# Performance work log

Measured on AMD Instinct MI355X. Metric: run time of the kernel, lower is better.

The kernel has to match this reference:

```python
import jax, jax.numpy as jnp
import numpy as np

HIDDEN = 1024
HEADS = 16
HEAD_DIM = HIDDEN // HEADS


def setup_inputs() -> dict:
    key = jax.random.key(0)
    ks = jax.random.split(key, 11)
    B, S = 2, 2048
    s = 1.0 / np.sqrt(HIDDEN)
    return {
        "query": jax.random.normal(ks[0], (B, S, HIDDEN), jnp.float32),
        "key": jax.random.normal(ks[1], (B, S, HIDDEN), jnp.float32),
        "value": jax.random.normal(ks[2], (B, S, HIDDEN), jnp.float32),
        "Wq": jax.random.normal(ks[3], (HIDDEN, HIDDEN), jnp.float32) * s,
        "bq": jnp.zeros((HIDDEN,), jnp.float32),
        "Wk": jax.random.normal(ks[4], (HIDDEN, HIDDEN), jnp.float32) * s,
        "bk": jnp.zeros((HIDDEN,), jnp.float32),
        "Wv": jax.random.normal(ks[5], (HIDDEN, HIDDEN), jnp.float32) * s,
        "bv": jnp.zeros((HIDDEN,), jnp.float32),
        "Wo": jax.random.normal(ks[6], (HIDDEN, HIDDEN), jnp.float32) * s,
        "bo": jnp.zeros((HIDDEN,), jnp.float32),
    }


def reference(query, key, value, Wq, bq, Wk, bk, Wv, bv, Wo, bo):
    B, S, _ = query.shape
    # QKV projections (torch Linear: x @ W.T + b)
    Q = query @ Wq.T + bq
    K = key @ Wk.T + bk
    V = value @ Wv.T + bv
    # split heads: [B, S, H, D] -> [B, H, S, D]
    Q = Q.reshape(B, S, HEADS, HEAD_DIM).transpose(0, 2, 1, 3)
    K = K.reshape(B, S, HEADS, HEAD_DIM).transpose(0, 2, 1, 3)
    V = V.reshape(B, S, HEADS, HEAD_DIM).transpose(0, 2, 1, 3)
    scale = jnp.sqrt(jnp.float32(HEAD_DIM))
    # energy = Q K^T / sqrt(d)  -> [B, H, Sq, Sk]
    energy = jnp.einsum("bhqd,bhkd->bhqk", Q, K) / scale
    attn = jax.nn.softmax(energy, axis=-1)
    # dropout p=0.0 in eval -> identity
    x = jnp.einsum("bhqk,bhkd->bhqd", attn, V)
    x = x.transpose(0, 2, 1, 3).reshape(B, S, HIDDEN)
    return x @ Wo.T + bo
```

## Files before the change

### kernel.cpp

```cpp
#include <hip/hip_runtime.h>

typedef __attribute__((ext_vector_type(8))) short short8;
typedef __attribute__((ext_vector_type(4))) float f32x4;
typedef __attribute__((ext_vector_type(16))) float f32x16;

#define SEQ 2048
#define NB 2
#define HID 1024
#define NH 16
#define HD 64
#define MS (NB * SEQ)

#define QSCALE 0.18033688011112042f

typedef const __attribute__((address_space(1))) unsigned int* gptr_t;
typedef __attribute__((address_space(3))) unsigned int* lptr_t;

__device__ inline ushort f2bf(float f) {
  union { float f; unsigned u; } x; x.f = f;
  unsigned r = x.u + 0x7fffu + ((x.u >> 16) & 1u);
  return (ushort)(r >> 16);
}

__device__ __forceinline__ unsigned cvt_pk_bf16(float lo, float hi) {
  unsigned r;
  asm("v_cvt_pk_bf16_f32 %0, %1, %2" : "=v"(r) : "v"(lo), "v"(hi));
  return r;
}

__global__ void cast3(const float* __restrict__ a, const float* __restrict__ b,
                      const float* __restrict__ c, ushort* __restrict__ oa,
                      ushort* __restrict__ ob, ushort* __restrict__ oc, int n4) {
  const int z = blockIdx.y;
  const float* in = (z == 0) ? a : (z == 1) ? b : c;
  ushort* out = (z == 0) ? oa : (z == 1) ? ob : oc;
  int i = blockIdx.x * 256 + threadIdx.x;
  if (i >= n4) return;
  float4 v = reinterpret_cast<const float4*>(in)[i];
  ushort4 o;
  o.x = f2bf(v.x); o.y = f2bf(v.y); o.z = f2bf(v.z); o.w = f2bf(v.w);
  reinterpret_cast<ushort4*>(out)[i] = o;
}

__global__ void cast4(const float* __restrict__ a, const float* __restrict__ b,
                      const float* __restrict__ c, const float* __restrict__ d,
                      ushort* __restrict__ oa, ushort* __restrict__ ob,
                      ushort* __restrict__ oc, ushort* __restrict__ od, int n4) {
  const int z = blockIdx.y;
  const float* in = (z == 0) ? a : (z == 1) ? b : (z == 2) ? c : d;
  ushort* out = (z == 0) ? oa : (z == 1) ? ob : (z == 2) ? oc : od;
  int i = blockIdx.x * 256 + threadIdx.x;
  if (i >= n4) return;
  float4 v = reinterpret_cast<const float4*>(in)[i];
  ushort4 o;
  o.x = f2bf(v.x); o.y = f2bf(v.y); o.z = f2bf(v.z); o.w = f2bf(v.w);
  reinterpret_cast<ushort4*>(out)[i] = o;
}

template <int BN, int OUT>
__device__ __forceinline__ void gemm_body(const ushort* __restrict__ A,
                                          const ushort* __restrict__ B,
                                          const float* __restrict__ bias,
                                          void* __restrict__ Out,
                                          ushort* As, ushort* Bs) {
  constexpr int NJ = BN / 32;
  const int tid = threadIdx.x;
  const int wave = tid >> 6, lane = tid & 63;
  const int lr = lane & 15, lg = lane >> 4;
  const int wr = wave >> 1, wc = wave & 1;
  const int bm = blockIdx.y, bn = blockIdx.x;

  f32x4 acc[4][NJ];
#pragma unroll
  for (int i = 0; i < 4; ++i)
#pragma unroll
    for (int j = 0; j < NJ; ++j) acc[i][j] = (f32x4)(0.f);

  const int l4 = lane >> 2;
  const int lc = (lane & 3) * 8;

  for (int k0 = 0; k0 < HID; k0 += 32) {
#pragma unroll
    for (int c = 0; c < 2; ++c) {
      const int chunk = wave * 2 + c;
      const ushort* ga = &A[(size_t)(bm * 128 + chunk * 16 + l4) * HID + k0 + lc];
      __builtin_amdgcn_global_load_lds((gptr_t)(const void*)ga, (lptr_t)(void*)&As[chunk * 512], 16, 0, 0);
    }
    if (BN == 128) {
#pragma unroll
      for (int c = 0; c < 2; ++c) {
        const int chunk = wave * 2 + c;
        const ushort* gb = &B[(size_t)(bn * BN + chunk * 16 + l4) * HID + k0 + lc];
        __builtin_amdgcn_global_load_lds((gptr_t)(const void*)gb, (lptr_t)(void*)&Bs[chunk * 512], 16, 0, 0);
      }
    } else {
      const ushort* gb = &B[(size_t)(bn * BN + wave * 16 + l4) * HID + k0 + lc];
      __builtin_amdgcn_global_load_lds((gptr_t)(const void*)gb, (lptr_t)(void*)&Bs[wave * 512], 16, 0, 0);
    }
    __syncthreads();
    short8 af[4], bf[NJ];
#pragma unroll
    for (int i = 0; i < 4; ++i)
      af[i] = *reinterpret_cast<const short8*>(&As[(wr * 64 + i * 16 + lr) * 32 + lg * 8]);
#pragma unroll
    for (int j = 0; j < NJ; ++j)
      bf[j] = *reinterpret_cast<const short8*>(&Bs[(wc * (BN / 2) + j * 16 + lr) * 32 + lg * 8]);
#pragma unroll
    for (int i = 0; i < 4; ++i)
#pragma unroll
      for (int j = 0; j < NJ; ++j)
        acc[i][j] = __builtin_amdgcn_mfma_f32_16x16x32_bf16(af[i], bf[j], acc[i][j], 0, 0, 0);
    __syncthreads();
  }

#pragma unroll
  for (int i = 0; i < 4; ++i)
#pragma unroll
    for (int j = 0; j < NJ; ++j) {
      const int row0 = bm * 128 + wr * 64 + i * 16 + lg * 4;
      const int col = bn * BN + wc * (BN / 2) + j * 16 + lr;
      const float bv = bias[col];
#pragma unroll
      for (int r = 0; r < 4; ++r) {
        float v = acc[i][j][r] + bv;
        if (OUT == 0)
          ((float*)Out)[(size_t)(row0 + r) * HID + col] = v;
        else if (OUT == 1)
          ((ushort*)Out)[(size_t)(row0 + r) * HID + col] = f2bf(v);
        else
          ((ushort*)Out)[(size_t)(row0 + r) * HID + col] = f2bf(v * QSCALE);
      }
    }
}

__global__ __launch_bounds__(256) void gemm_qkv(const ushort* __restrict__ A0, const ushort* __restrict__ A1,
                                                const ushort* __restrict__ A2, const ushort* __restrict__ W0,
                                                const ushort* __restrict__ W1, const ushort* __restrict__ W2,
                                                const float* __restrict__ b0, const float* __restrict__ b1,
                                                const float* __restrict__ b2, ushort* __restrict__ O0,
                                                ushort* __restrict__ O1, ushort* __restrict__ O2) {
  __shared__ alignas(16) ushort As[128 * 32];
  __shared__ alignas(16) ushort Bs[128 * 32];
  const int z = blockIdx.z;
  if (z == 0)      gemm_body<128, 2>(A0, W0, b0, O0, As, Bs);
  else if (z == 1) gemm_body<128, 1>(A1, W1, b1, O1, As, Bs);
  else             gemm_body<128, 1>(A2, W2, b2, O2, As, Bs);
}

__global__ __launch_bounds__(256) void gemm_wo(const ushort* __restrict__ A, const ushort* __restrict__ W,
                                               const float* __restrict__ bias, float* __restrict__ O) {
  __shared__ alignas(16) ushort As[128 * 32];
  __shared__ alignas(16) ushort Bs[64 * 32];
  gemm_body<64, 0>(A, W, bias, O, As, Bs);
}

__global__ __launch_bounds__(256) void vt_kernel(const ushort* __restrict__ Vp, ushort* __restrict__ VT) {
  __shared__ ushort Lt[64][68];
  const int sb = blockIdx.x, bh = blockIdx.y;
  const int b = bh >> 4, h = bh & 15;
  const int t = threadIdx.x;
  const int s4 = (t & 15) * 4, d4 = (t >> 4) * 4;
  ushort v[4][4];
#pragma unroll
  for (int r = 0; r < 4; ++r) {
    ushort4 x = *reinterpret_cast<const ushort4*>(
        &Vp[(size_t)(b * SEQ + sb * 64 + s4 + r) * HID + h * 64 + d4]);
    v[r][0] = x.x; v[r][1] = x.y; v[r][2] = x.z; v[r][3] = x.w;
  }
#pragma unroll
  for (int j = 0; j < 4; ++j) {
    ushort4 y; y.x = v[0][j]; y.y = v[1][j]; y.z = v[2][j]; y.w = v[3][j];
    *reinterpret_cast<ushort4*>(&Lt[d4 + j][s4]) = y;
  }
  __syncthreads();
  const int dl = t >> 2, s0 = (t & 3) * 16;
  ushort4 o[4];
#pragma unroll
  for (int p = 0; p < 4; ++p) o[p] = *reinterpret_cast<const ushort4*>(&Lt[dl][s0 + p * 4]);
  ushort* dst = &VT[((size_t)bh * HD + dl) * SEQ + sb * 64 + s0];
#pragma unroll
  for (int p = 0; p < 4; ++p) *reinterpret_cast<ushort4*>(&dst[p * 4]) = o[p];
}

__device__ __forceinline__ short8 ldfrag(const char* tb, int r, int g) {
  return *reinterpret_cast<const short8*>(tb + r * 128 + ((g * 16) ^ ((r & 7) << 4)));
}

__global__ __launch_bounds__(512, 4) void attn_kernel(const ushort* __restrict__ Q,
                                                      const ushort* __restrict__ Kp,
                                                      const ushort* __restrict__ VT,
                                                      ushort* __restrict__ Op) {
  __shared__ alignas(16) ushort lds[32768];

  const int bh = blockIdx.x;
  const int b = bh >> 4, h = bh & 15;
  const int qt = blockIdx.y;
  const int tid = threadIdx.x;
  const int w = tid >> 6, lane = tid & 63;
  const int q = lane & 31, hi = lane >> 5;
  const int qsub = w & 3, chf = w >> 2;

  const size_t base = (size_t)b * SEQ * HID + h * HD;
  const size_t vtbase = (size_t)bh * HD * SEQ;

  const int qrow = qt * 128 + qsub * 32 + q;
  short8 qf[4];
#pragma unroll
  for (int s = 0; s < 4; ++s)
    qf[s] = *reinterpret_cast<const short8*>(&Q[base + (size_t)qrow * HID + s * 16 + hi * 8]);

  f32x16 acc0 = (f32x16)(0.f), acc1 = (f32x16)(0.f);
  float mrun = -3e38f;
  float ps0 = 0.f, ps1 = 0.f, ps2 = 0.f, ps3 = 0.f;

  const int tsel = w >> 1, part = w & 1, sh = tsel & 1;
  const bool isK = tsel < 2;
  const int r8 = lane >> 3;
  const int sx = ((lane & 7) ^ r8) * 8;

  auto stage = [&](int buf, int ktb) {
    const int kt = ktb + sh * 16;
#pragma unroll
    for (int c = 0; c < 4; ++c) {
      const int G = part * 4 + c, r = G * 8 + r8;
      const ushort* src;
      ushort* dst;
      if (isK) {
        src = &Kp[base + (size_t)(kt * 64 + r) * HID + sx];
        dst = &lds[(sh * 2 + buf) * 4096 + G * 512];
      } else {
        src = &VT[vtbase + (size_t)r * SEQ + kt * 64 + sx];
        dst = &lds[16384 + (sh * 2 + buf) * 4096 + G * 512];
      }
      __builtin_amdgcn_global_load_lds((gptr_t)(const void*)src, (lptr_t)(void*)dst, 16, 0, 0);
    }
  };

  auto mkfrag = [&](const unsigned* Wg) -> short8 {
    unsigned X0 = (unsigned)__shfl_xor((int)Wg[0], 32, 64);
    unsigned X1 = (unsigned)__shfl_xor((int)Wg[1], 32, 64);
    unsigned X2 = (unsigned)__shfl_xor((int)Wg[2], 32, 64);
    unsigned X3 = (unsigned)__shfl_xor((int)Wg[3], 32, 64);
    union { unsigned u[4]; short8 v; } p;
    p.u[0] = hi ? X2 : Wg[0];
    p.u[1] = hi ? X3 : Wg[1];
    p.u[2] = hi ? Wg[2] : X0;
    p.u[3] = hi ? Wg[3] : X1;
    return p.v;
  };

  stage(0, 0);
  __syncthreads();

  int buf = 0;
  for (int ktb = 0; ktb < 16; ++ktb) {
    stage(buf ^ 1, (ktb + 1) & 15);

    const char* kb = (const char*)lds + (chf * 2 + buf) * 8192;
    const char* vb = (const char*)lds + 32768 + (chf * 2 + buf) * 8192;

    f32x16 s0 = (f32x16)(0.f), s1 = (f32x16)(0.f);
#pragma unroll
    for (int cs = 0; cs < 4; ++cs) {
      short8 a = ldfrag(kb, q, cs * 2 + hi);
      s0 = __builtin_amdgcn_mfma_f32_32x32x16_bf16(a, qf[cs], s0, 0, 0, 0);
    }
#pragma unroll
    for (int cs = 0; cs < 4; ++cs) {
      short8 a = ldfrag(kb, 32 + q, cs * 2 + hi);
      s1 = __builtin_amdgcn_mfma_f32_32x32x16_bf16(a, qf[cs], s1, 0, 0, 0);
    }

    float t8[8];
#pragma unroll
    for (int i = 0; i < 8; ++i)
      t8[i] = fmaxf(fmaxf(s0[i], s0[i + 8]), fmaxf(s1[i], s1[i + 8]));
    float pm = fmaxf(fmaxf(fmaxf(t8[0], t8[4]), fmaxf(t8[1], t8[5])),
                     fmaxf(fmaxf(t8[2], t8[6]), fmaxf(t8[3], t8[7])));
    pm = fmaxf(pm, __shfl_xor(pm, 32, 64));
    if (__any(pm > mrun + 8.f)) {
      const float mnew = fmaxf(mrun, pm);
      const float corr = __builtin_amdgcn_exp2f(mrun - mnew);
      mrun = mnew;
      ps0 *= corr; ps1 *= corr; ps2 *= corr; ps3 *= corr;
#pragma unroll
      for (int i = 0; i < 16; ++i) { acc0[i] *= corr; acc1[i] *= corr; }
    }
#pragma unroll
    for (int i = 0; i < 16; ++i) {
      s0[i] = __builtin_amdgcn_exp2f(s0[i] - mrun);
      s1[i] = __builtin_amdgcn_exp2f(s1[i] - mrun);
    }
    float a8[8];
#pragma unroll
    for (int i = 0; i < 8; ++i) a8[i] = (s0[i] + s0[i + 8]) + (s1[i] + s1[i + 8]);
    ps0 += a8[0] + a8[4]; ps1 += a8[1] + a8[5];
    ps2 += a8[2] + a8[6]; ps3 += a8[3] + a8[7];

    {
      unsigned W[8];
#pragma unroll
      for (int i = 0; i < 8; ++i) W[i] = cvt_pk_bf16(s0[2 * i], s0[2 * i + 1]);
      short8 p0 = mkfrag(W);
      short8 p1 = mkfrag(W + 4);
      short8 vf;
      vf = ldfrag(vb, q,      0 + hi); acc0 = __builtin_amdgcn_mfma_f32_32x32x16_bf16(vf, p0, acc0, 0, 0, 0);
      vf = ldfrag(vb, 32 + q, 0 + hi); acc1 = __builtin_amdgcn_mfma_f32_32x32x16_bf16(vf, p0, acc1, 0, 0, 0);
      vf = ldfrag(vb, q,      2 + hi); acc0 = __builtin_amdgcn_mfma_f32_32x32x16_bf16(vf, p1, acc0, 0, 0, 0);
      vf = ldfrag(vb, 32 + q, 2 + hi); acc1 = __builtin_amdgcn_mfma_f32_32x32x16_bf16(vf, p1, acc1, 0, 0, 0);
    }
    {
      unsigned W[8];
#pragma unroll
      for (int i = 0; i < 8; ++i) W[i] = cvt_pk_bf16(s1[2 * i], s1[2 * i + 1]);
      short8 p0 = mkfrag(W);
      short8 p1 = mkfrag(W + 4);
      short8 vf;
      vf = ldfrag(vb, q,      4 + hi); acc0 = __builtin_amdgcn_mfma_f32_32x32x16_bf16(vf, p0, acc0, 0, 0, 0);
      vf = ldfrag(vb, 32 + q, 4 + hi); acc1 = __builtin_amdgcn_mfma_f32_32x32x16_bf16(vf, p0, acc1, 0, 0, 0);
      vf = ldfrag(vb, q,      6 + hi); acc0 = __builtin_amdgcn_mfma_f32_32x32x16_bf16(vf, p1, acc0, 0, 0, 0);
      vf = ldfrag(vb, 32 + q, 6 + hi); acc1 = __builtin_amdgcn_mfma_f32_32x32x16_bf16(vf, p1, acc1, 0, 0, 0);
    }
    __syncthreads();
    buf ^= 1;
  }

  float lsum = (ps0 + ps1) + (ps2 + ps3);
  const float lfull = lsum + __shfl_xor(lsum, 32, 64);

  __syncthreads();
  float* fl = (float*)lds;
  const int p = w & 3;
  float* ob = fl + p * 2048 + lane * 32;
  if (w >= 4) {
#pragma unroll
    for (int i = 0; i < 4; ++i) {
      f32x4 x = {acc0[4 * i], acc0[4 * i + 1], acc0[4 * i + 2], acc0[4 * i + 3]};
      *reinterpret_cast<f32x4*>(ob + 4 * (i ^ (lane & 7))) = x;
    }
#pragma unroll
    for (int i = 0; i < 4; ++i) {
      f32x4 x = {acc1[4 * i], acc1[4 * i + 1], acc1[4 * i + 2], acc1[4 * i + 3]};
      *reinterpret_cast<f32x4*>(ob + 4 * ((i + 4) ^ (lane & 7))) = x;
    }
    fl[8192 + (p * 64 + lane) * 2] = mrun;
    fl[8192 + (p * 64 + lane) * 2 + 1] = lfull;
  }
  __syncthreads();
  if (w < 4) {
    const float m1 = fl[8192 + (p * 64 + lane) * 2];
    const float l1 = fl[8192 + (p * 64 + lane) * 2 + 1];
    float o1[32];
#pragma unroll
    for (int s = 0; s < 8; ++s) {
      f32x4 x = *reinterpret_cast<const f32x4*>(ob + 4 * (s ^ (lane & 7)));
      o1[4 * s] = x[0]; o1[4 * s + 1] = x[1]; o1[4 * s + 2] = x[2]; o1[4 * s + 3] = x[3];
    }
    const float mnew = fmaxf(mrun, m1);
    const float c0 = __builtin_amdgcn_exp2f(mrun - mnew);
    const float c1 = __builtin_amdgcn_exp2f(m1 - mnew);
    const float linv = 1.f / (lfull * c0 + l1 * c1);
#pragma unroll
    for (int g = 0; g < 4; ++g) {
      {
        float x0 = (acc0[4 * g + 0] * c0 + o1[4 * g + 0] * c1) * linv;
        float x1 = (acc0[4 * g + 1] * c0 + o1[4 * g + 1] * c1) * linv;
        float x2 = (acc0[4 * g + 2] * c0 + o1[4 * g + 2] * c1) * linv;
        float x3 = (acc0[4 * g + 3] * c0 + o1[4 * g + 3] * c1) * linv;
        uint2 wd; wd.x = cvt_pk_bf16(x0, x1); wd.y = cvt_pk_bf16(x2, x3);
        *reinterpret_cast<uint2*>(&Op[base + (size_t)qrow * HID + g * 8 + hi * 4]) = wd;
      }
      {
        float x0 = (acc1[4 * g + 0] * c0 + o1[16 + 4 * g + 0] * c1) * linv;
        float x1 = (acc1[4 * g + 1] * c0 + o1[16 + 4 * g + 1] * c1) * linv;
        float x2 = (acc1[4 * g + 2] * c0 + o1[16 + 4 * g + 2] * c1) * linv;
        float x3 = (acc1[4 * g + 3] * c0 + o1[16 + 4 * g + 3] * c1) * linv;
        uint2 wd; wd.x = cvt_pk_bf16(x0, x1); wd.y = cvt_pk_bf16(x2, x3);
        *reinterpret_cast<uint2*>(&Op[base + (size_t)qrow * HID + 32 + g * 8 + hi * 4]) = wd;
      }
    }
  }
}

extern "C" void kernel_launch(void* const* d_in, const int* in_sizes, int n_in,
                              void* d_out, int out_size, void* d_ws, size_t ws_size,
                              hipStream_t stream) {
  const float* query = (const float*)d_in[0];
  const float* key   = (const float*)d_in[1];
  const float* value = (const float*)d_in[2];
  const float* Wq = (const float*)d_in[3];
  const float* bq = (const float*)d_in[4];
  const float* Wk = (const float*)d_in[5];
  const float* bk = (const float*)d_in[6];
  const float* Wv = (const float*)d_in[7];
  const float* bv = (const float*)d_in[8];
  const float* Wo = (const float*)d_in[9];
  const float* bo = (const float*)d_in[10];

  const size_t actElems = (size_t)MS * HID;
  const size_t wElems = (size_t)HID * HID;
  char* ws = (char*)d_ws;
  ushort* qb = (ushort*)(ws + 0);
  ushort* kb = (ushort*)(ws + actElems * 2);
  ushort* vb = (ushort*)(ws + actElems * 4);
  ushort* wq = (ushort*)(ws + actElems * 6);
  ushort* wk = (ushort*)(ws + actElems * 6 + wElems * 2);
  ushort* wv = (ushort*)(ws + actElems * 6 + wElems * 4);
  ushort* wo = (ushort*)(ws + actElems * 6 + wElems * 6);
  ushort* Qp   = (ushort*)(ws + actElems * 6 + wElems * 8);
  ushort* Kp   = (ushort*)(ws + actElems * 8 + wElems * 8);
  ushort* VTp  = (ushort*)(ws + actElems * 10 + wElems * 8);
  ushort* XB   = (ushort*)(ws + actElems * 12 + wElems * 8);

  dim3 cg3((unsigned)(actElems / 4 / 256), 3);
  cast3<<<cg3, 256, 0, stream>>>(query, key, value, qb, kb, vb, (int)(actElems / 4));
  dim3 cg4((unsigned)(wElems / 4 / 256), 4);
  cast4<<<cg4, 256, 0, stream>>>(Wq, Wk, Wv, Wo, wq, wk, wv, wo, (int)(wElems / 4));

  dim3 gq(HID / 128, MS / 128, 3);
  gemm_qkv<<<gq, 256, 0, stream>>>(qb, kb, vb, wq, wk, wv, bq, bk, bv, Qp, Kp, XB);

  dim3 gv(SEQ / 64, NB * NH);
  vt_kernel<<<gv, 256, 0, stream>>>(XB, VTp);

  dim3 ga(NB * NH, SEQ / 128);
  attn_kernel<<<ga, 512, 0, stream>>>(Qp, Kp, VTp, XB);

  dim3 go(HID / 64, MS / 128);
  gemm_wo<<<go, 256, 0, stream>>>(XB, wo, bo, (float*)d_out);
}
```

Baseline: 251.5 us.

## Fuse cast kernels, write V transposed from GEMM epilogue, XCD-aware block swizzle

The two fp32-to-bf16 cast kernels are merged into one launch. The V projection epilogue now writes straight into the head-transposed VT layout with packed bf16 stores, so the separate transpose kernel and its extra pass over V are removed. Both GEMMs also remap block indices so that blocks landing on the same XCD share row tiles, aiming for better L2 reuse. The transposed epilogue stores are strided rather than row-contiguous, which may reduce write coalescing.

```diff
diff --git a/kernel.cpp b/kernel.cpp
--- a/kernel.cpp
+++ b/kernel.cpp
@@ -28,32 +28,30 @@
   return r;
 }
 
-__global__ void cast3(const float* __restrict__ a, const float* __restrict__ b,
-                      const float* __restrict__ c, ushort* __restrict__ oa,
-                      ushort* __restrict__ ob, ushort* __restrict__ oc, int n4) {
-  const int z = blockIdx.y;
-  const float* in = (z == 0) ? a : (z == 1) ? b : c;
-  ushort* out = (z == 0) ? oa : (z == 1) ? ob : oc;
-  int i = blockIdx.x * 256 + threadIdx.x;
-  if (i >= n4) return;
-  float4 v = reinterpret_cast<const float4*>(in)[i];
+__global__ __launch_bounds__(256) void cast_all(
+    const float* __restrict__ q, const float* __restrict__ k, const float* __restrict__ v,
+    const float* __restrict__ w0, const float* __restrict__ w1, const float* __restrict__ w2,
+    const float* __restrict__ w3, ushort* __restrict__ oq, ushort* __restrict__ ok,
+    ushort* __restrict__ ov, ushort* __restrict__ o0, ushort* __restrict__ o1,
+    ushort* __restrict__ o2, ushort* __restrict__ o3) {
+  const int id = blockIdx.x;
+  const float* in;
+  ushort* out;
+  int i;
+  if (id < 12288) {
+    const int z = id >> 12;
+    in = (z == 0) ? q : (z == 1) ? k : v;
+    out = (z == 0) ? oq : (z == 1) ? ok : ov;
+    i = (id & 4095) * 256 + threadIdx.x;
+  } else {
+    const int z = (id - 12288) >> 10;
+    in = (z == 0) ? w0 : (z == 1) ? w1 : (z == 2) ? w2 : w3;
+    out = (z == 0) ? o0 : (z == 1) ? o1 : (z == 2) ? o2 : o3;
+    i = ((id - 12288) & 1023) * 256 + threadIdx.x;
+  }
+  float4 vv = reinterpret_cast<const float4*>(in)[i];
   ushort4 o;
-  o.x = f2bf(v.x); o.y = f2bf(v.y); o.z = f2bf(v.z); o.w = f2bf(v.w);
-  reinterpret_cast<ushort4*>(out)[i] = o;
-}
-
-__global__ void cast4(const float* __restrict__ a, const float* __restrict__ b,
-                      const float* __restrict__ c, const float* __restrict__ d,
-                      ushort* __restrict__ oa, ushort* __restrict__ ob,
-                      ushort* __restrict__ oc, ushort* __restrict__ od, int n4) {
-  const int z = blockIdx.y;
-  const float* in = (z == 0) ? a : (z == 1) ? b : (z == 2) ? c : d;
-  ushort* out = (z == 0) ? oa : (z == 1) ? ob : (z == 2) ? oc : od;
-  int i = blockIdx.x * 256 + threadIdx.x;
-  if (i >= n4) return;
-  float4 v = reinterpret_cast<const float4*>(in)[i];
-  ushort4 o;
-  o.x = f2bf(v.x); o.y = f2bf(v.y); o.z = f2bf(v.z); o.w = f2bf(v.w);
+  o.x = f2bf(vv.x); o.y = f2bf(vv.y); o.z = f2bf(vv.z); o.w = f2bf(vv.w);
   reinterpret_cast<ushort4*>(out)[i] = o;
 }
 
@@ -62,13 +60,12 @@
                                           const ushort* __restrict__ B,
                                           const float* __restrict__ bias,
                                           void* __restrict__ Out,
-                                          ushort* As, ushort* Bs) {
+                                          ushort* As, ushort* Bs, int bm, int bn) {
   constexpr int NJ = BN / 32;
   const int tid = threadIdx.x;
   const int wave = tid >> 6, lane = tid & 63;
   const int lr = lane & 15, lg = lane >> 4;
   const int wr = wave >> 1, wc = wave & 1;
-  const int bm = blockIdx.y, bn = blockIdx.x;
 
   f32x4 acc[4][NJ];
 #pragma unroll
@@ -120,15 +117,24 @@
       const int row0 = bm * 128 + wr * 64 + i * 16 + lg * 4;
       const int col = bn * BN + wc * (BN / 2) + j * 16 + lr;
       const float bv = bias[col];
-#pragma unroll
-      for (int r = 0; r < 4; ++r) {
-        float v = acc[i][j][r] + bv;
-        if (OUT == 0)
-          ((float*)Out)[(size_t)(row0 + r) * HID + col] = v;
-        else if (OUT == 1)
-          ((ushort*)Out)[(size_t)(row0 + r) * HID + col] = f2bf(v);
-        else
-          ((ushort*)Out)[(size_t)(row0 + r) * HID + col] = f2bf(v * QSCALE);
+      if (OUT == 3) {
+        uint2 w;
+        w.x = cvt_pk_bf16(acc[i][j][0] + bv, acc[i][j][1] + bv);
+        w.y = cvt_pk_bf16(acc[i][j][2] + bv, acc[i][j][3] + bv);
+        size_t off = ((size_t)((row0 >> 11) * NH + (col >> 6)) << 17) +
+                     ((size_t)(col & 63) << 11) + (size_t)(row0 & 2047);
+        *reinterpret_cast<uint2*>(&((ushort*)Out)[off]) = w;
+      } else {
+#pragma unroll
+        for (int r = 0; r < 4; ++r) {
+          float v = acc[i][j][r] + bv;
+          if (OUT == 0)
+            ((float*)Out)[(size_t)(row0 + r) * HID + col] = v;
+          else if (OUT == 1)
+            ((ushort*)Out)[(size_t)(row0 + r) * HID + col] = f2bf(v);
+          else
+            ((ushort*)Out)[(size_t)(row0 + r) * HID + col] = f2bf(v * QSCALE);
+        }
       }
     }
 }
@@ -141,45 +147,25 @@
                                                 ushort* __restrict__ O1, ushort* __restrict__ O2) {
   __shared__ alignas(16) ushort As[128 * 32];
   __shared__ alignas(16) ushort Bs[128 * 32];
+  const int f = blockIdx.y * 8 + blockIdx.x;
+  const int xcd = f & 7, slot = f >> 3;
+  const int bm = xcd * 4 + (slot >> 3);
+  const int bn = slot & 7;
   const int z = blockIdx.z;
-  if (z == 0)      gemm_body<128, 2>(A0, W0, b0, O0, As, Bs);
-  else if (z == 1) gemm_body<128, 1>(A1, W1, b1, O1, As, Bs);
-  else             gemm_body<128, 1>(A2, W2, b2, O2, As, Bs);
+  if (z == 0)      gemm_body<128, 2>(A0, W0, b0, O0, As, Bs, bm, bn);
+  else if (z == 1) gemm_body<128, 1>(A1, W1, b1, O1, As, Bs, bm, bn);
+  else             gemm_body<128, 3>(A2, W2, b2, O2, As, Bs, bm, bn);
 }
 
 __global__ __launch_bounds__(256) void gemm_wo(const ushort* __restrict__ A, const ushort* __restrict__ W,
                                                const float* __restrict__ bias, float* __restrict__ O) {
   __shared__ alignas(16) ushort As[128 * 32];
   __shared__ alignas(16) ushort Bs[64 * 32];
-  gemm_body<64, 0>(A, W, bias, O, As, Bs);
-}
-
-__global__ __launch_bounds__(256) void vt_kernel(const ushort* __restrict__ Vp, ushort* __restrict__ VT) {
-  __shared__ ushort Lt[64][68];
-  const int sb = blockIdx.x, bh = blockIdx.y;
-  const int b = bh >> 4, h = bh & 15;
-  const int t = threadIdx.x;
-  const int s4 = (t & 15) * 4, d4 = (t >> 4) * 4;
-  ushort v[4][4];
-#pragma unroll
-  for (int r = 0; r < 4; ++r) {
-    ushort4 x = *reinterpret_cast<const ushort4*>(
-        &Vp[(size_t)(b * SEQ + sb * 64 + s4 + r) * HID + h * 64 + d4]);
-    v[r][0] = x.x; v[r][1] = x.y; v[r][2] = x.z; v[r][3] = x.w;
-  }
-#pragma unroll
-  for (int j = 0; j < 4; ++j) {
-    ushort4 y; y.x = v[0][j]; y.y = v[1][j]; y.z = v[2][j]; y.w = v[3][j];
-    *reinterpret_cast<ushort4*>(&Lt[d4 + j][s4]) = y;
-  }
-  __syncthreads();
-  const int dl = t >> 2, s0 = (t & 3) * 16;
-  ushort4 o[4];
-#pragma unroll
-  for (int p = 0; p < 4; ++p) o[p] = *reinterpret_cast<const ushort4*>(&Lt[dl][s0 + p * 4]);
-  ushort* dst = &VT[((size_t)bh * HD + dl) * SEQ + sb * 64 + s0];
-#pragma unroll
-  for (int p = 0; p < 4; ++p) *reinterpret_cast<ushort4*>(&dst[p * 4]) = o[p];
+  const int f = blockIdx.y * 16 + blockIdx.x;
+  const int xcd = f & 7, slot = f >> 3;
+  const int bm = xcd * 4 + (slot >> 4);
+  const int bn = slot & 15;
+  gemm_body<64, 0>(A, W, bias, O, As, Bs, bm, bn);
 }
 
 __device__ __forceinline__ short8 ldfrag(const char* tb, int r, int g) {
@@ -412,20 +398,15 @@
   ushort* VTp  = (ushort*)(ws + actElems * 10 + wElems * 8);
   ushort* XB   = (ushort*)(ws + actElems * 12 + wElems * 8);
 
-  dim3 cg3((unsigned)(actElems / 4 / 256), 3);
-  cast3<<<cg3, 256, 0, stream>>>(query, key, value, qb, kb, vb, (int)(actElems / 4));
-  dim3 cg4((unsigned)(wElems / 4 / 256), 4);
-  cast4<<<cg4, 256, 0, stream>>>(Wq, Wk, Wv, Wo, wq, wk, wv, wo, (int)(wElems / 4));
-
-  dim3 gq(HID / 128, MS / 128, 3);
-  gemm_qkv<<<gq, 256, 0, stream>>>(qb, kb, vb, wq, wk, wv, bq, bk, bv, Qp, Kp, XB);
-
-  dim3 gv(SEQ / 64, NB * NH);
-  vt_kernel<<<gv, 256, 0, stream>>>(XB, VTp);
+  cast_all<<<16384, 256, 0, stream>>>(query, key, value, Wq, Wk, Wv, Wo,
+                                      qb, kb, vb, wq, wk, wv, wo);
+
+  dim3 gq(8, 32, 3);
+  gemm_qkv<<<gq, 256, 0, stream>>>(qb, kb, vb, wq, wk, wv, bq, bk, bv, Qp, Kp, VTp);
 
   dim3 ga(NB * NH, SEQ / 128);
   attn_kernel<<<ga, 512, 0, stream>>>(Qp, Kp, VTp, XB);
 
-  dim3 go(HID / 64, MS / 128);
+  dim3 go(16, 32);
   gemm_wo<<<go, 256, 0, stream>>>(XB, wo, bo, (float*)d_out);
 }
```

New measurement: 237.3 us. -5.6%, faster.
